# Kernel optimization log

Hardware: AMD Instinct MI355X
Metric: run time of the kernel (lower is better)

Reference implementation:

```python
import jax, jax.numpy as jnp
import numpy as np

D_IN, D_OUT, K = 256, 512, 64
X_MIN, X_MAX = 0.0, 1.0
EPS = 1e-12


def pchip_slopes(y, x):
    """Fritsch-Carlson PCHIP slopes along last dim. y:(...,K), x:(K,) -> (...,K)."""
    h = x[1:] - x[:-1]                                  # (K-1,)
    delta = (y[..., 1:] - y[..., :-1]) / (h + EPS)      # (...,K-1)

    def limit(di, de):
        di = jnp.where(di * de <= 0, jnp.zeros_like(di), di)
        return jnp.where(jnp.abs(di) > 3 * jnp.abs(de), 3 * de, di)

    d0 = ((2 * h[0] + h[1]) * delta[..., 0] - h[0] * delta[..., 1]) / (h[0] + h[1] + EPS)
    dN = ((2 * h[-1] + h[-2]) * delta[..., -1] - h[-1] * delta[..., -2]) / (h[-1] + h[-2] + EPS)
    dp, dn = delta[..., :-1], delta[..., 1:]
    same_sign = dp * dn > 0
    w1 = 2 * h[1:] + h[:-1]
    w2 = h[1:] + 2 * h[:-1]
    d_int = (w1 + w2) / (w1 / (dp + EPS) + w2 / (dn + EPS) + EPS)
    mid = jnp.where(same_sign, d_int, jnp.zeros_like(d_int))
    return jnp.concatenate([limit(d0, delta[..., 0])[..., None], mid,
                            limit(dN, delta[..., -1])[..., None]], axis=-1)


def kan_forward(x, coeffs, bias, knots):
    """x:(B,d_in), coeffs:(d_out,d_in,K), bias:(d_out,), knots:(K,) -> (B,d_out)."""
    Kn = knots.shape[0]
    d = pchip_slopes(coeffs, knots)                     # (d_out,d_in,K)

    xc = jnp.clip(x, knots[0], knots[-1])
    idx = jnp.clip(jnp.searchsorted(knots, xc) - 1, 0, Kn - 2)   # (B,d_in)
    x0 = knots[idx]
    h = knots[idx + 1] - x0 + EPS
    t = (xc - x0) / h
    t2 = t * t
    t3 = t2 * t
    h00 = 2 * t3 - 3 * t2 + 1
    h10 = t3 - 2 * t2 + t
    h01 = -2 * t3 + 3 * t2
    h11 = t3 - t2

    below = x < knots[0]
    above = x > knots[-1]
    ext = below | above
    # linear extrapolation: value = y_edge + d_edge * (x - knot_edge)
    k0 = jnp.where(below, 0, jnp.where(above, Kn - 1, idx))
    k1 = jnp.where(ext, k0, idx + 1)                    # dummy (zero-weight) index when extrapolating
    dx_ext = jnp.where(below, x - knots[0], x - knots[-1])
    a_y0 = jnp.where(ext, jnp.ones_like(h00), h00)
    a_y1 = jnp.where(ext, jnp.zeros_like(h01), h01)
    a_d0 = jnp.where(ext, dx_ext, h10 * h)
    a_d1 = jnp.where(ext, jnp.zeros_like(h11), h11 * h)

    oh0 = jax.nn.one_hot(k0, Kn, dtype=x.dtype)         # (B,d_in,K)
    oh1 = jax.nn.one_hot(k1, Kn, dtype=x.dtype)
    Wy = a_y0[..., None] * oh0 + a_y1[..., None] * oh1  # weights applied to knot values
    Wd = a_d0[..., None] * oh0 + a_d1[..., None] * oh1  # weights applied to knot slopes

    out = (jnp.einsum('bik,oik->bo', Wy, coeffs)
           + jnp.einsum('bik,oik->bo', Wd, d)
           + bias[None, :])
    return out


def setup_inputs() -> dict:
    key = jax.random.key(0)
    k1, k2 = jax.random.split(key)
    B = 4096
    x = jax.random.uniform(k1, (B, D_IN), dtype=jnp.float32)
    init_scale = 0.1 / np.sqrt(D_IN)
    coeffs = jax.random.normal(k2, (D_OUT, D_IN, K), dtype=jnp.float32) * init_scale
    bias = jnp.zeros((D_OUT,), dtype=jnp.float32)
    knots = jnp.linspace(X_MIN, X_MAX, K, dtype=jnp.float32)
    return {"x": x, "coeffs": coeffs, "bias": bias, "knots": knots}


def reference(x, coeffs, bias, knots):
    return kan_forward(x, coeffs, bias, knots)
```

## Files before the change

### kernel.cpp

```cpp
#include <hip/hip_runtime.h>
#include <hip/hip_fp16.h>
#include <cstdint>

#define D_IN   256
#define D_OUT  512
#define KK     64
#define BATCH  4096
#define EPSF   1e-12f

#define NCH    4
#define CI     (D_IN / NCH)
#define BT     128


using half2v = _Float16 __attribute__((ext_vector_type(2)));

__device__ __forceinline__ float dot2(uint32_t a, uint32_t b, float c) {
#if defined(__has_builtin) && __has_builtin(__builtin_amdgcn_fdot2)
  return __builtin_amdgcn_fdot2(__builtin_bit_cast(half2v, a),
                                __builtin_bit_cast(half2v, b), c, false);
#else
  __half2 ah = __builtin_bit_cast(__half2, a);
  __half2 bh = __builtin_bit_cast(__half2, b);
  return c + __half2float(ah.x) * __half2float(bh.x)
           + __half2float(ah.y) * __half2float(bh.y);
#endif
}

__device__ __forceinline__ uint32_t packh2(float a, float b) {
  __half2 h = __floats2half2_rn(a, b);
  return __builtin_bit_cast(uint32_t, h);
}


__global__ __launch_bounds__(256)
void kan_pack(const float* __restrict__ coeffs,
              const float* __restrict__ knots,
              uint32_t* __restrict__ pk2p) {
  __shared__ float s_kn[KK];
  __shared__ float s_h[KK];
  int tid = threadIdx.x;
  if (tid < KK) s_kn[tid] = knots[tid];
  __syncthreads();
  if (tid < KK - 1) s_h[tid] = s_kn[tid + 1] - s_kn[tid];
  __syncthreads();

  int o = blockIdx.x * 256 + tid;
  int i = blockIdx.y;
  const float* C = coeffs + ((size_t)o * D_IN + i) * KK;

  float c[KK];
#pragma unroll
  for (int k = 0; k < KK; k += 4) {
    float4 v = *(const float4*)(C + k);
    c[k] = v.x; c[k + 1] = v.y; c[k + 2] = v.z; c[k + 3] = v.w;
  }

  float d[KK];
  float h0 = s_h[0], h1 = s_h[1];
  float del0 = (c[1] - c[0]) / (h0 + EPSF);
  float del1 = (c[2] - c[1]) / (h1 + EPSF);
  {
    float di = ((2.f * h0 + h1) * del0 - h0 * del1) / (h0 + h1 + EPSF);
    di = (di * del0 <= 0.f) ? 0.f : di;
    di = (fabsf(di) > 3.f * fabsf(del0)) ? 3.f * del0 : di;
    d[0] = di;
  }
  float dp = del0, dn = del1;
#pragma unroll
  for (int k = 1; k <= KK - 2; ++k) {
    float hk = s_h[k], hkm = s_h[k - 1];
    float w1 = 2.f * hk + hkm;
    float w2 = hk + 2.f * hkm;
    float dint = (w1 + w2) / (w1 / (dp + EPSF) + w2 / (dn + EPSF) + EPSF);
    d[k] = (dp * dn > 0.f) ? dint : 0.f;
    if (k < KK - 2) {
      float nd = (c[k + 2] - c[k + 1]) / (s_h[k + 1] + EPSF);
      dp = dn; dn = nd;
    }
  }
  {
    float hN = s_h[KK - 2], hNm = s_h[KK - 3];
    float di = ((2.f * hN + hNm) * dn - hN * dp) / (hN + hNm + EPSF);
    di = (di * dn <= 0.f) ? 0.f : di;
    di = (fabsf(di) > 3.f * fabsf(dn)) ? 3.f * dn : di;
    d[KK - 1] = di;
  }

  const int oq = o >> 7, og = o & 127;
#pragma unroll
  for (int k = 0; k < KK; ++k) {
    float hk = ((k < KK - 1) ? s_h[k] : s_h[KK - 2]) + EPSF;
    pk2p[((size_t)(((i << 2) + oq) << 6) + k) * 128 + og] = packh2(c[k], d[k] * hk);
  }
}


__global__ __launch_bounds__(512)
void kan_w(const float* __restrict__ x, uint2* __restrict__ W8,
           unsigned char* __restrict__ K0) {
  const int i = blockIdx.x;
  const float inv63 = 1.0f / 63.0f;
  for (int b = threadIdx.x; b < BATCH; b += 512) {
    float xv = x[(size_t)b * D_IN + i];
    float xc = fminf(fmaxf(xv, 0.f), 1.f);
    int k0 = (int)(xc * 63.0f);
    k0 = min(k0, KK - 2);
    float x0 = (float)k0 * inv63;
    if (xc < x0)                              { k0--; x0 -= inv63; }
    else if (k0 < KK - 2 && xc >= x0 + inv63) { k0++; x0 += inv63; }
    float t  = (xc - x0) * 63.0f;
    float t2 = t * t;
    float t3 = t2 * t;
    float wy0 = 2.f * t3 - 3.f * t2 + 1.f;
    float wy1 = 3.f * t2 - 2.f * t3;
    float wd0 = t3 - 2.f * t2 + t;
    float wd1 = t3 - t2;
    uint2 w;
    w.x = packh2(wy0, wd0);
    w.y = packh2(wy1, wd1);
    W8[(size_t)i * BATCH + b] = w;
    K0[(size_t)i * BATCH + b] = (unsigned char)k0;
  }
}


__global__ __launch_bounds__(512, 4)
void kan_main(const uint2* __restrict__ W8, const unsigned char* __restrict__ K0,
              const uint4* __restrict__ pkq, __half* __restrict__ P) {
  __shared__ uint4 sb[2][2048];

  const int bid   = blockIdx.x;
  const int chunk = bid & 3;
  const int rest  = bid >> 2;
  const int oq    = rest & 3;
  const int btile = rest >> 2;
  const int tid   = threadIdx.x;
  const int g     = tid & 31;
  const int s     = tid >> 5;
  const int bbase = btile * BT + s * 8;
  const int i0    = chunk * CI;

  float acc[8][4];
#pragma unroll
  for (int j = 0; j < 8; ++j)
#pragma unroll
    for (int m = 0; m < 4; ++m) acc[j][m] = 0.f;

  uint4 wreg[4];
  uint64_t k8;
  {
    const uint4* wp = (const uint4*)(W8 + (size_t)i0 * BATCH + bbase);
#pragma unroll
    for (int n = 0; n < 4; ++n) wreg[n] = wp[n];
    k8 = *(const uint64_t*)(K0 + (size_t)i0 * BATCH + bbase);
  }
  {
    const uint4* src = pkq + ((size_t)((i0 << 2) + oq) << 11);
    uint4 r0 = src[tid], r1 = src[tid + 512], r2 = src[tid + 1024], r3 = src[tid + 1536];
    sb[0][tid] = r0; sb[0][tid + 512] = r1; sb[0][tid + 1024] = r2; sb[0][tid + 1536] = r3;
  }
  __syncthreads();

  for (int ic = 0; ic < CI; ++ic) {
    const int cur = ic & 1;
    const int i   = i0 + ic;
    const bool more = (ic + 1 < CI);

    uint4 r0, r1, r2, r3, wnxt[4];
    uint64_t k8n = 0;
    if (more) {
      const uint4* src = pkq + ((size_t)(((i + 1) << 2) + oq) << 11);
      r0 = src[tid]; r1 = src[tid + 512]; r2 = src[tid + 1024]; r3 = src[tid + 1536];
      const uint4* wp = (const uint4*)(W8 + (size_t)(i + 1) * BATCH + bbase);
#pragma unroll
      for (int n = 0; n < 4; ++n) wnxt[n] = wp[n];
      k8n = *(const uint64_t*)(K0 + (size_t)(i + 1) * BATCH + bbase);
    }

    const uint4* bufc = sb[cur];
#pragma unroll
    for (int j = 0; j < 8; ++j) {
      const uint32_t k0 = (uint32_t)(k8 >> (8 * j)) & 0xFFu;
      const uint4* p = bufc + k0 * 32 + g;
      uint4 q0 = p[0];
      uint4 q1 = p[32];
      uint4 t  = wreg[j >> 1];
      uint32_t w0 = (j & 1) ? t.z : t.x;
      uint32_t w1 = (j & 1) ? t.w : t.y;
      acc[j][0] = dot2(q0.x, w0, acc[j][0]); acc[j][0] = dot2(q1.x, w1, acc[j][0]);
      acc[j][1] = dot2(q0.y, w0, acc[j][1]); acc[j][1] = dot2(q1.y, w1, acc[j][1]);
      acc[j][2] = dot2(q0.z, w0, acc[j][2]); acc[j][2] = dot2(q1.z, w1, acc[j][2]);
      acc[j][3] = dot2(q0.w, w0, acc[j][3]); acc[j][3] = dot2(q1.w, w1, acc[j][3]);
    }

    if (more) {
      uint4* bufn = sb[cur ^ 1];
      bufn[tid] = r0; bufn[tid + 512] = r1; bufn[tid + 1024] = r2; bufn[tid + 1536] = r3;
#pragma unroll
      for (int n = 0; n < 4; ++n) wreg[n] = wnxt[n];
      k8 = k8n;
    }
    __syncthreads();
  }

  const size_t pb = ((size_t)chunk * BATCH + bbase) * D_OUT + oq * 128 + g * 4;
#pragma unroll
  for (int j = 0; j < 8; ++j) {
    uint2 h;
    h.x = packh2(acc[j][0], acc[j][1]);
    h.y = packh2(acc[j][2], acc[j][3]);
    *(uint2*)((char*)P + (pb + (size_t)j * D_OUT) * 2) = h;
  }
}


__global__ __launch_bounds__(256)
void kan_reduce(const __half* __restrict__ P, const float* __restrict__ bias,
                float* __restrict__ out) {
  const size_t t = (size_t)blockIdx.x * 256 + threadIdx.x;
  const int o4 = (int)(t & 127);
  float4 sum = ((const float4*)bias)[o4];
#pragma unroll
  for (int c = 0; c < NCH; ++c) {
    uint2 h = *(const uint2*)((const char*)P +
              ((size_t)c * BATCH * D_OUT + t * 4) * 2);
    __half2 h01 = __builtin_bit_cast(__half2, h.x);
    __half2 h23 = __builtin_bit_cast(__half2, h.y);
    sum.x += __half2float(h01.x); sum.y += __half2float(h01.y);
    sum.z += __half2float(h23.x); sum.w += __half2float(h23.y);
  }
  ((float4*)out)[t] = sum;
}


extern "C" void kernel_launch(void* const* d_in, const int* in_sizes, int n_in,
                              void* d_out, int out_size, void* d_ws, size_t ws_size,
                              hipStream_t stream) {
  const float* x      = (const float*)d_in[0];
  const float* coeffs = (const float*)d_in[1];
  const float* bias   = (const float*)d_in[2];
  const float* knots  = (const float*)d_in[3];
  float* out = (float*)d_out;

  const size_t pk_bytes = (size_t)D_IN * KK * D_OUT * 4;
  const size_t w_bytes  = (size_t)D_IN * BATCH * 8;
  const size_t k_bytes  = (size_t)D_IN * BATCH;
  const size_t p_bytes  = (size_t)NCH * BATCH * D_OUT * 2;
  if (ws_size < pk_bytes + w_bytes + k_bytes + p_bytes) return;

  char* ws = (char*)d_ws;
  uint32_t*      pk2p = (uint32_t*)ws;
  uint2*         W8   = (uint2*)(ws + pk_bytes);
  unsigned char* K0   = (unsigned char*)(ws + pk_bytes + w_bytes);
  __half*        P    = (__half*)(ws + pk_bytes + w_bytes + k_bytes);

  kan_pack<<<dim3(D_OUT / 256, D_IN), 256, 0, stream>>>(coeffs, knots, pk2p);
  kan_w   <<<D_IN, 512, 0, stream>>>(x, W8, K0);
  kan_main<<<dim3(NCH * 4 * (BATCH / BT)), 512, 0, stream>>>(W8, K0,
            (const uint4*)pk2p, P);
  kan_reduce<<<dim3(BATCH * D_OUT / 4 / 256), 256, 0, stream>>>(P, bias, out);
}
```

Baseline: 138.6 us.

## Merge prep kernels, widen main blocks to 1024 threads, split input dim eight ways

Folds the coefficient-packing and weight-computation kernels into a single launch. The main kernel grows to 1024 threads with a 256-row batch tile, so each shared-memory coefficient tile is reused by twice as many rows. When the workspace allows, the input dimension is split into 8 chunks instead of 4, which keeps the block count up. W8 is now loaded directly each iteration rather than register-prefetched, and the reduce kernel reads more fp16 partials. The cost is extra partial-sum traffic and possible occupancy limits from the larger blocks.

```diff
diff --git a/kernel.cpp b/kernel.cpp
--- a/kernel.cpp
+++ b/kernel.cpp
@@ -7,10 +7,7 @@
 #define KK     64
 #define BATCH  4096
 #define EPSF   1e-12f
-
-#define NCH    4
-#define CI     (D_IN / NCH)
-#define BT     128
+#define BT     256
 
 
 using half2v = _Float16 __attribute__((ext_vector_type(2)));
@@ -34,112 +31,114 @@
 
 
 __global__ __launch_bounds__(256)
-void kan_pack(const float* __restrict__ coeffs,
-              const float* __restrict__ knots,
-              uint32_t* __restrict__ pk2p) {
+void kan_prep(const float* __restrict__ coeffs, const float* __restrict__ knots,
+              const float* __restrict__ x,
+              uint32_t* __restrict__ pk2p, uint2* __restrict__ W8,
+              unsigned char* __restrict__ K0) {
   __shared__ float s_kn[KK];
   __shared__ float s_h[KK];
-  int tid = threadIdx.x;
-  if (tid < KK) s_kn[tid] = knots[tid];
-  __syncthreads();
-  if (tid < KK - 1) s_h[tid] = s_kn[tid + 1] - s_kn[tid];
-  __syncthreads();
-
-  int o = blockIdx.x * 256 + tid;
-  int i = blockIdx.y;
-  const float* C = coeffs + ((size_t)o * D_IN + i) * KK;
-
-  float c[KK];
-#pragma unroll
-  for (int k = 0; k < KK; k += 4) {
-    float4 v = *(const float4*)(C + k);
-    c[k] = v.x; c[k + 1] = v.y; c[k + 2] = v.z; c[k + 3] = v.w;
-  }
-
-  float d[KK];
-  float h0 = s_h[0], h1 = s_h[1];
-  float del0 = (c[1] - c[0]) / (h0 + EPSF);
-  float del1 = (c[2] - c[1]) / (h1 + EPSF);
-  {
-    float di = ((2.f * h0 + h1) * del0 - h0 * del1) / (h0 + h1 + EPSF);
-    di = (di * del0 <= 0.f) ? 0.f : di;
-    di = (fabsf(di) > 3.f * fabsf(del0)) ? 3.f * del0 : di;
-    d[0] = di;
-  }
-  float dp = del0, dn = del1;
-#pragma unroll
-  for (int k = 1; k <= KK - 2; ++k) {
-    float hk = s_h[k], hkm = s_h[k - 1];
-    float w1 = 2.f * hk + hkm;
-    float w2 = hk + 2.f * hkm;
-    float dint = (w1 + w2) / (w1 / (dp + EPSF) + w2 / (dn + EPSF) + EPSF);
-    d[k] = (dp * dn > 0.f) ? dint : 0.f;
-    if (k < KK - 2) {
-      float nd = (c[k + 2] - c[k + 1]) / (s_h[k + 1] + EPSF);
-      dp = dn; dn = nd;
-    }
-  }
-  {
-    float hN = s_h[KK - 2], hNm = s_h[KK - 3];
-    float di = ((2.f * hN + hNm) * dn - hN * dp) / (hN + hNm + EPSF);
-    di = (di * dn <= 0.f) ? 0.f : di;
-    di = (fabsf(di) > 3.f * fabsf(dn)) ? 3.f * dn : di;
-    d[KK - 1] = di;
-  }
-
-  const int oq = o >> 7, og = o & 127;
-#pragma unroll
-  for (int k = 0; k < KK; ++k) {
-    float hk = ((k < KK - 1) ? s_h[k] : s_h[KK - 2]) + EPSF;
-    pk2p[((size_t)(((i << 2) + oq) << 6) + k) * 128 + og] = packh2(c[k], d[k] * hk);
-  }
-}
-
-
-__global__ __launch_bounds__(512)
-void kan_w(const float* __restrict__ x, uint2* __restrict__ W8,
-           unsigned char* __restrict__ K0) {
-  const int i = blockIdx.x;
-  const float inv63 = 1.0f / 63.0f;
-  for (int b = threadIdx.x; b < BATCH; b += 512) {
-    float xv = x[(size_t)b * D_IN + i];
-    float xc = fminf(fmaxf(xv, 0.f), 1.f);
-    int k0 = (int)(xc * 63.0f);
-    k0 = min(k0, KK - 2);
-    float x0 = (float)k0 * inv63;
-    if (xc < x0)                              { k0--; x0 -= inv63; }
-    else if (k0 < KK - 2 && xc >= x0 + inv63) { k0++; x0 += inv63; }
-    float t  = (xc - x0) * 63.0f;
-    float t2 = t * t;
-    float t3 = t2 * t;
-    float wy0 = 2.f * t3 - 3.f * t2 + 1.f;
-    float wy1 = 3.f * t2 - 2.f * t3;
-    float wd0 = t3 - 2.f * t2 + t;
-    float wd1 = t3 - t2;
-    uint2 w;
-    w.x = packh2(wy0, wd0);
-    w.y = packh2(wy1, wd1);
-    W8[(size_t)i * BATCH + b] = w;
-    K0[(size_t)i * BATCH + b] = (unsigned char)k0;
-  }
-}
-
-
-__global__ __launch_bounds__(512, 4)
+  const int bid = blockIdx.x;
+  const int tid = threadIdx.x;
+
+  if (bid < 512) {
+    if (tid < KK) s_kn[tid] = knots[tid];
+    __syncthreads();
+    if (tid < KK - 1) s_h[tid] = s_kn[tid + 1] - s_kn[tid];
+    __syncthreads();
+
+    const int i = bid >> 1;
+    const int o = (bid & 1) * 256 + tid;
+    const float* C = coeffs + ((size_t)o * D_IN + i) * KK;
+
+    float c[KK];
+#pragma unroll
+    for (int k = 0; k < KK; k += 4) {
+      float4 v = *(const float4*)(C + k);
+      c[k] = v.x; c[k + 1] = v.y; c[k + 2] = v.z; c[k + 3] = v.w;
+    }
+
+    float d[KK];
+    float h0 = s_h[0], h1 = s_h[1];
+    float del0 = (c[1] - c[0]) / (h0 + EPSF);
+    float del1 = (c[2] - c[1]) / (h1 + EPSF);
+    {
+      float di = ((2.f * h0 + h1) * del0 - h0 * del1) / (h0 + h1 + EPSF);
+      di = (di * del0 <= 0.f) ? 0.f : di;
+      di = (fabsf(di) > 3.f * fabsf(del0)) ? 3.f * del0 : di;
+      d[0] = di;
+    }
+    float dp = del0, dn = del1;
+#pragma unroll
+    for (int k = 1; k <= KK - 2; ++k) {
+      float hk = s_h[k], hkm = s_h[k - 1];
+      float w1 = 2.f * hk + hkm;
+      float w2 = hk + 2.f * hkm;
+      float dint = (w1 + w2) / (w1 / (dp + EPSF) + w2 / (dn + EPSF) + EPSF);
+      d[k] = (dp * dn > 0.f) ? dint : 0.f;
+      if (k < KK - 2) {
+        float nd = (c[k + 2] - c[k + 1]) / (s_h[k + 1] + EPSF);
+        dp = dn; dn = nd;
+      }
+    }
+    {
+      float hN = s_h[KK - 2], hNm = s_h[KK - 3];
+      float di = ((2.f * hN + hNm) * dn - hN * dp) / (hN + hNm + EPSF);
+      di = (di * dn <= 0.f) ? 0.f : di;
+      di = (fabsf(di) > 3.f * fabsf(dn)) ? 3.f * dn : di;
+      d[KK - 1] = di;
+    }
+
+    const int oq = o >> 7, og = o & 127;
+#pragma unroll
+    for (int k = 0; k < KK; ++k) {
+      float hk = ((k < KK - 1) ? s_h[k] : s_h[KK - 2]) + EPSF;
+      pk2p[((size_t)(((i << 2) + oq) << 6) + k) * 128 + og] = packh2(c[k], d[k] * hk);
+    }
+  } else {
+    const int i = bid - 512;
+    const float inv63 = 1.0f / 63.0f;
+    for (int b = tid; b < BATCH; b += 256) {
+      float xv = x[(size_t)b * D_IN + i];
+      float xc = fminf(fmaxf(xv, 0.f), 1.f);
+      int k0 = (int)(xc * 63.0f);
+      k0 = min(k0, KK - 2);
+      float x0 = (float)k0 * inv63;
+      if (xc < x0)                              { k0--; x0 -= inv63; }
+      else if (k0 < KK - 2 && xc >= x0 + inv63) { k0++; x0 += inv63; }
+      float t  = (xc - x0) * 63.0f;
+      float t2 = t * t;
+      float t3 = t2 * t;
+      float wy0 = 2.f * t3 - 3.f * t2 + 1.f;
+      float wy1 = 3.f * t2 - 2.f * t3;
+      float wd0 = t3 - 2.f * t2 + t;
+      float wd1 = t3 - t2;
+      uint2 w;
+      w.x = packh2(wy0, wd0);
+      w.y = packh2(wy1, wd1);
+      W8[(size_t)i * BATCH + b] = w;
+      K0[(size_t)i * BATCH + b] = (unsigned char)k0;
+    }
+  }
+}
+
+
+template<int LG>
+__global__ __launch_bounds__(1024, 8)
 void kan_main(const uint2* __restrict__ W8, const unsigned char* __restrict__ K0,
               const uint4* __restrict__ pkq, __half* __restrict__ P) {
   __shared__ uint4 sb[2][2048];
 
+  const int CIk   = D_IN >> LG;
   const int bid   = blockIdx.x;
-  const int chunk = bid & 3;
-  const int rest  = bid >> 2;
+  const int chunk = bid & ((1 << LG) - 1);
+  const int rest  = bid >> LG;
   const int oq    = rest & 3;
   const int btile = rest >> 2;
   const int tid   = threadIdx.x;
   const int g     = tid & 31;
   const int s     = tid >> 5;
   const int bbase = btile * BT + s * 8;
-  const int i0    = chunk * CI;
+  const int i0    = chunk * CIk;
 
   float acc[8][4];
 #pragma unroll
@@ -147,36 +146,31 @@
 #pragma unroll
     for (int m = 0; m < 4; ++m) acc[j][m] = 0.f;
 
-  uint4 wreg[4];
-  uint64_t k8;
-  {
-    const uint4* wp = (const uint4*)(W8 + (size_t)i0 * BATCH + bbase);
-#pragma unroll
-    for (int n = 0; n < 4; ++n) wreg[n] = wp[n];
-    k8 = *(const uint64_t*)(K0 + (size_t)i0 * BATCH + bbase);
-  }
+  uint64_t k8 = *(const uint64_t*)(K0 + (size_t)i0 * BATCH + bbase);
   {
     const uint4* src = pkq + ((size_t)((i0 << 2) + oq) << 11);
-    uint4 r0 = src[tid], r1 = src[tid + 512], r2 = src[tid + 1024], r3 = src[tid + 1536];
-    sb[0][tid] = r0; sb[0][tid + 512] = r1; sb[0][tid + 1024] = r2; sb[0][tid + 1536] = r3;
+    uint4 r0 = src[tid], r1 = src[tid + 1024];
+    sb[0][tid] = r0; sb[0][tid + 1024] = r1;
   }
   __syncthreads();
 
-  for (int ic = 0; ic < CI; ++ic) {
+  for (int ic = 0; ic < CIk; ++ic) {
     const int cur = ic & 1;
     const int i   = i0 + ic;
-    const bool more = (ic + 1 < CI);
-
-    uint4 r0, r1, r2, r3, wnxt[4];
+    const bool more = (ic + 1 < CIk);
+
+    uint4 r0, r1;
     uint64_t k8n = 0;
     if (more) {
       const uint4* src = pkq + ((size_t)(((i + 1) << 2) + oq) << 11);
-      r0 = src[tid]; r1 = src[tid + 512]; r2 = src[tid + 1024]; r3 = src[tid + 1536];
-      const uint4* wp = (const uint4*)(W8 + (size_t)(i + 1) * BATCH + bbase);
-#pragma unroll
-      for (int n = 0; n < 4; ++n) wnxt[n] = wp[n];
+      r0 = src[tid]; r1 = src[tid + 1024];
       k8n = *(const uint64_t*)(K0 + (size_t)(i + 1) * BATCH + bbase);
     }
+
+    uint4 wreg[4];
+    const uint4* wp = (const uint4*)(W8 + (size_t)i * BATCH + bbase);
+#pragma unroll
+    for (int n = 0; n < 4; ++n) wreg[n] = wp[n];
 
     const uint4* bufc = sb[cur];
 #pragma unroll
@@ -196,9 +190,7 @@
 
     if (more) {
       uint4* bufn = sb[cur ^ 1];
-      bufn[tid] = r0; bufn[tid + 512] = r1; bufn[tid + 1024] = r2; bufn[tid + 1536] = r3;
-#pragma unroll
-      for (int n = 0; n < 4; ++n) wreg[n] = wnxt[n];
+      bufn[tid] = r0; bufn[tid + 1024] = r1;
       k8 = k8n;
     }
     __syncthreads();
@@ -217,12 +209,11 @@
 
 __global__ __launch_bounds__(256)
 void kan_reduce(const __half* __restrict__ P, const float* __restrict__ bias,
-                float* __restrict__ out) {
+                float* __restrict__ out, int nchunk) {
   const size_t t = (size_t)blockIdx.x * 256 + threadIdx.x;
   const int o4 = (int)(t & 127);
   float4 sum = ((const float4*)bias)[o4];
-#pragma unroll
-  for (int c = 0; c < NCH; ++c) {
+  for (int c = 0; c < nchunk; ++c) {
     uint2 h = *(const uint2*)((const char*)P +
               ((size_t)c * BATCH * D_OUT + t * 4) * 2);
     __half2 h01 = __builtin_bit_cast(__half2, h.x);
@@ -246,18 +237,24 @@
   const size_t pk_bytes = (size_t)D_IN * KK * D_OUT * 4;
   const size_t w_bytes  = (size_t)D_IN * BATCH * 8;
   const size_t k_bytes  = (size_t)D_IN * BATCH;
-  const size_t p_bytes  = (size_t)NCH * BATCH * D_OUT * 2;
-  if (ws_size < pk_bytes + w_bytes + k_bytes + p_bytes) return;
+  const size_t fixed    = pk_bytes + w_bytes + k_bytes;
+  const size_t p_one    = (size_t)BATCH * D_OUT * 2;
+
+  int lg = 3;
+  if (ws_size < fixed + (p_one << 3)) lg = 2;
+  if (ws_size < fixed + (p_one << lg)) return;
+  const int nchunk = 1 << lg;
 
   char* ws = (char*)d_ws;
   uint32_t*      pk2p = (uint32_t*)ws;
   uint2*         W8   = (uint2*)(ws + pk_bytes);
   unsigned char* K0   = (unsigned char*)(ws + pk_bytes + w_bytes);
-  __half*        P    = (__half*)(ws + pk_bytes + w_bytes + k_bytes);
-
-  kan_pack<<<dim3(D_OUT / 256, D_IN), 256, 0, stream>>>(coeffs, knots, pk2p);
-  kan_w   <<<D_IN, 512, 0, stream>>>(x, W8, K0);
-  kan_main<<<dim3(NCH * 4 * (BATCH / BT)), 512, 0, stream>>>(W8, K0,
-            (const uint4*)pk2p, P);
-  kan_reduce<<<dim3(BATCH * D_OUT / 4 / 256), 256, 0, stream>>>(P, bias, out);
-}
+  __half*        P    = (__half*)(ws + fixed);
+
+  kan_prep<<<dim3(768), 256, 0, stream>>>(coeffs, knots, x, pk2p, W8, K0);
+  if (lg == 3)
+    kan_main<3><<<dim3(16 * 4 * 8), 1024, 0, stream>>>(W8, K0, (const uint4*)pk2p, P);
+  else
+    kan_main<2><<<dim3(16 * 4 * 4), 1024, 0, stream>>>(W8, K0, (const uint4*)pk2p, P);
+  kan_reduce<<<dim3(BATCH * D_OUT / 4 / 256), 256, 0, stream>>>(P, bias, out, nchunk);
+}
```

Measured after the change: 126.6 us. 8.6% less time.
